# Performance work log

Hardware: AMD Instinct MI355X
Metric: run time of the kernel (lower is better)

The kernel has to match this reference:

```python
import jax, jax.numpy as jnp
import numpy as np

# MLA config (must match init_kwargs)
D_MODEL = 2048
NUM_HEADS = 16
HEAD_DIM = D_MODEL // NUM_HEADS          # 128
D_LATENT = 512
D_QK = D_LATENT // 2                      # 256
D_V = D_LATENT - D_QK                     # 256
ROPE_DIM = 64
QK_DEC = HEAD_DIM - ROPE_DIM              # 64
B, S = 2, 2048


def _glorot(key, shape):
    lim = np.sqrt(6.0 / (shape[0] + shape[1]))
    return jax.random.uniform(key, shape, jnp.float32, -lim, lim)


def setup_inputs() -> dict:
    key = jax.random.key(0)
    ks = jax.random.split(key, 8)
    return {
        "x": jax.random.normal(ks[0], (B, S, D_MODEL), jnp.float32),
        "W_comp": _glorot(ks[1], (D_MODEL, D_LATENT)),
        "W_q_dec": _glorot(ks[2], (D_QK, NUM_HEADS * QK_DEC)),
        "W_k_dec": _glorot(ks[3], (D_QK, NUM_HEADS * QK_DEC)),
        "W_v_dec": _glorot(ks[4], (D_V, NUM_HEADS * HEAD_DIM)),
        "W_rope_q": _glorot(ks[5], (D_MODEL, NUM_HEADS * ROPE_DIM)),
        "W_rope_k": _glorot(ks[6], (D_MODEL, NUM_HEADS * ROPE_DIM)),
        "W_out": _glorot(ks[7], (D_MODEL, D_MODEL)),
    }


def _apply_rope(t):
    # t: [B, S, H, ROPE_DIM]; rotate-half formulation with base 10000
    half = ROPE_DIM // 2
    inv_freq = 1.0 / (10000.0 ** (jnp.arange(0, ROPE_DIM, 2, dtype=jnp.float32) / ROPE_DIM))
    ang = jnp.arange(t.shape[1], dtype=jnp.float32)[:, None] * inv_freq[None, :]  # [S, half]
    cos = jnp.cos(ang)[None, :, None, :]
    sin = jnp.sin(ang)[None, :, None, :]
    t1, t2 = t[..., :half], t[..., half:]
    return jnp.concatenate([t1 * cos - t2 * sin, t1 * sin + t2 * cos], axis=-1)


def reference(x, W_comp, W_q_dec, W_k_dec, W_v_dec, W_rope_q, W_rope_k, W_out):
    # Compress to shared latent [B,S,d_latent]
    compressed = jnp.einsum("bsd,dl->bsl", x, W_comp)
    c_qk = compressed[:, :, :D_QK]
    c_v = compressed[:, :, D_QK:]

    # Decompress content parts and project RoPE parts from raw input
    q_no_rope = jnp.einsum("bsl,lh->bsh", c_qk, W_q_dec)   # [B,S,H*QK_DEC]
    k_no_rope = jnp.einsum("bsl,lh->bsh", c_qk, W_k_dec)
    v = jnp.einsum("bsl,lh->bsh", c_v, W_v_dec).reshape(B, S, NUM_HEADS, HEAD_DIM)
    q_rope = jnp.einsum("bsd,dh->bsh", x, W_rope_q)        # [B,S,H*ROPE_DIM]
    k_rope = jnp.einsum("bsd,dh->bsh", x, W_rope_k)

    # Faithful to source: concat along flat feature dim, then reshape to heads
    q = jnp.concatenate([q_no_rope, q_rope], axis=-1).reshape(B, S, NUM_HEADS, HEAD_DIM)
    k = jnp.concatenate([k_no_rope, k_rope], axis=-1).reshape(B, S, NUM_HEADS, HEAD_DIM)

    # Apply RoPE to last ROPE_DIM dims of each head
    q = jnp.concatenate([q[..., :QK_DEC], _apply_rope(q[..., QK_DEC:])], axis=-1)
    k = jnp.concatenate([k[..., :QK_DEC], _apply_rope(k[..., QK_DEC:])], axis=-1)

    scale = 1.0 / jnp.sqrt(jnp.float32(HEAD_DIM))
    scores = jnp.einsum("bqhd,bkhd->bhqk", q, k) * scale   # [B,H,S,S]
    attn = jax.nn.softmax(scores, axis=-1)
    ctx = jnp.einsum("bhqk,bkhd->bqhd", attn, v).reshape(B, S, D_MODEL)
    return jnp.einsum("bsd,de->bse", ctx, W_out)
```

## Files before the change

### kernel.cpp

```cpp
#include <hip/hip_runtime.h>
#include <stdint.h>

typedef __bf16 bf16x8 __attribute__((ext_vector_type(8)));
typedef __bf16 bf16x4 __attribute__((ext_vector_type(4)));
typedef float f32x4 __attribute__((ext_vector_type(4)));
typedef float f32x16 __attribute__((ext_vector_type(16)));

constexpr int NB   = 2;
constexpr int SEQ  = 2048;
constexpr int DM   = 2048;
constexpr int NH   = 16;
constexpr int HD   = 128;
constexpr int DL   = 512;
constexpr int ROWS = NB * SEQ;

__device__ __forceinline__ void gload16(const void* g, void* l) {
  __builtin_amdgcn_global_load_lds((const __attribute__((address_space(1))) uint32_t*)(const void*)g,
                                   (__attribute__((address_space(3))) uint32_t*)(void*)l, 16, 0, 0);
}

__device__ __forceinline__ uint32_t pk2(float lo, float hi) {
  union { __bf16 h[2]; uint32_t u; } x;
  x.h[0] = (__bf16)lo; x.h[1] = (__bf16)hi;
  return x.u;
}

__global__ __launch_bounds__(256) void cast_bf16(const float* __restrict__ in,
                                                 __bf16* __restrict__ out, int n4) {
  int i = blockIdx.x * blockDim.x + threadIdx.x;
  int stride = gridDim.x * blockDim.x;
  for (int k = i; k < n4; k += stride) {
    float4 v = ((const float4*)in)[k];
    union { __bf16 h[4]; uint2 u; } uo;
    uo.h[0] = (__bf16)v.x; uo.h[1] = (__bf16)v.y;
    uo.h[2] = (__bf16)v.z; uo.h[3] = (__bf16)v.w;
    ((uint2*)out)[k] = uo.u;
  }
}

__global__ __launch_bounds__(256) void transpose_cast(const float* __restrict__ in,
                                                      __bf16* __restrict__ out,
                                                      int R, int C) {
  __shared__ float t[32][33];
  int r0 = blockIdx.y * 32, c0 = blockIdx.x * 32;
  int tx = threadIdx.x, ty = threadIdx.y;
#pragma unroll
  for (int i = 0; i < 4; ++i)
    t[ty + 8*i][tx] = in[(size_t)(r0 + ty + 8*i) * C + c0 + tx];
  __syncthreads();
#pragma unroll
  for (int i = 0; i < 4; ++i)
    out[(size_t)(c0 + ty + 8*i) * R + r0 + tx] = (__bf16)t[tx][ty + 8*i];
}

__global__ __launch_bounds__(256) void transpose_v(const __bf16* __restrict__ v,
                                                   __bf16* __restrict__ vt) {
  __shared__ __bf16 t[32][33];
  int b = blockIdx.z >> 4, h = blockIdx.z & 15;
  int s0 = blockIdx.x * 32, d0 = blockIdx.y * 32;
  int tx = threadIdx.x, ty = threadIdx.y;
#pragma unroll
  for (int i = 0; i < 4; ++i)
    t[ty + 8*i][tx] = v[(size_t)(b*SEQ + s0 + ty + 8*i) * 2048 + h*128 + d0 + tx];
  __syncthreads();
#pragma unroll
  for (int i = 0; i < 4; ++i)
    vt[((size_t)(b*NH + h) * 128 + d0 + ty + 8*i) * 2048 + s0 + tx] = t[tx][ty + 8*i];
}

template <typename CT>
__global__ __launch_bounds__(256) void gemm_bt(const __bf16* __restrict__ A, int lda,
                                               const __bf16* __restrict__ Bt, int ldb,
                                               CT* __restrict__ C, int ldc, int K_) {
  __shared__ __align__(16) __bf16 As[128 * 32];
  __shared__ __align__(16) __bf16 Bs[128 * 32];
  const int m0 = blockIdx.y * 128, n0 = blockIdx.x * 128;
  const int t = threadIdx.x;
  const int wid = t >> 6, lane = t & 63;
  const int wr = (wid >> 1) * 64, wc = (wid & 1) * 64;
  const int lr = lane & 15, lg = lane >> 4;
  f32x4 acc[4][4] = {};
  for (int k0 = 0; k0 < K_; k0 += 32) {
    __syncthreads();
#pragma unroll
    for (int j = 0; j < 2; ++j) {
      int ob = j * 4096 + wid * 1024;
      int o  = ob + lane * 16;
      int row = o >> 6, colb = o & 63;
      gload16((const char*)A  + ((size_t)(m0 + row) * lda + k0) * 2 + colb, (char*)As + ob);
      gload16((const char*)Bt + ((size_t)(n0 + row) * ldb + k0) * 2 + colb, (char*)Bs + ob);
    }
    __syncthreads();
    bf16x8 af[4], bfr[4];
#pragma unroll
    for (int mi = 0; mi < 4; ++mi)
      af[mi] = *(const bf16x8*)(As + (wr + mi*16 + lr) * 32 + 8*lg);
#pragma unroll
    for (int ni = 0; ni < 4; ++ni)
      bfr[ni] = *(const bf16x8*)(Bs + (wc + ni*16 + lr) * 32 + 8*lg);
#pragma unroll
    for (int mi = 0; mi < 4; ++mi)
#pragma unroll
      for (int ni = 0; ni < 4; ++ni)
        acc[mi][ni] = __builtin_amdgcn_mfma_f32_16x16x32_bf16(af[mi], bfr[ni], acc[mi][ni], 0, 0, 0);
  }
#pragma unroll
  for (int mi = 0; mi < 4; ++mi)
#pragma unroll
    for (int ni = 0; ni < 4; ++ni) {
      int r = m0 + wr + mi*16 + lg*4;
      int c = n0 + wc + ni*16 + lr;
#pragma unroll
      for (int j = 0; j < 4; ++j)
        C[(size_t)(r + j) * ldc + c] = (CT)acc[mi][ni][j];
    }
}

__global__ __launch_bounds__(64) void rope_assemble(const __bf16* __restrict__ nr,
                                                    const __bf16* __restrict__ rp,
                                                    __bf16* __restrict__ full) {
  int idx = blockIdx.x;
  int h = idx & 15, bs = idx >> 4;
  int s = bs & (SEQ - 1);
  int j = threadIdx.x;
  const size_t ibase = (size_t)bs * 1024;
  const size_t obase = (size_t)bs * 2048 + h * 128;
  auto get = [&](int d) -> float {
    int flat = h * 128 + d;
    return (flat < 1024) ? (float)nr[ibase + flat] : (float)rp[ibase + flat - 1024];
  };
  full[obase + j] = (__bf16)get(j);
  if (j < 32) {
    float t1 = get(64 + j), t2 = get(96 + j);
    float inv = exp2f(-0.41524101186092029f * (float)j);
    float ang = (float)s * inv;
    float sn, cs;
    sincosf(ang, &sn, &cs);
    full[obase + 64 + j] = (__bf16)(t1 * cs - t2 * sn);
    full[obase + 96 + j] = (__bf16)(t1 * sn + t2 * cs);
  }
}

__global__ __launch_bounds__(256, 2) void attn_fwd(const __bf16* __restrict__ qf,
                                                   const __bf16* __restrict__ kf,
                                                   const __bf16* __restrict__ vt,
                                                   __bf16* __restrict__ ctx) {
  __shared__ __align__(16) char Ks[2][16384];
  __shared__ __align__(16) char Vs[2][16384];
  const int t = threadIdx.x;
  const int wid = t >> 6, lane = t & 63;
  const int lq = lane & 31, hi = lane >> 5;
  const int h = blockIdx.y, b = blockIdx.z;
  const int qrow = blockIdx.x * 128 + wid * 32 + lq;
  const char* kbh = (const char*)(kf + (size_t)b * SEQ * DM + h * HD);
  const char* vbh = (const char*)(vt + (size_t)(b * NH + h) * HD * SEQ);

  bf16x8 qfr[8];
  const __bf16* qrp = qf + (size_t)(b * SEQ + qrow) * DM + h * HD;
#pragma unroll
  for (int kk = 0; kk < 8; ++kk)
    qfr[kk] = *(const bf16x8*)(qrp + kk * 16 + 8 * hi);

  f32x16 accO[4] = {};
  float mrun = -1e30f, lsum = 0.f;
  const float scale = 0.088388347648318447f;

  auto stageK = [&](int buf, int kc) {
#pragma unroll
    for (int i = 0; i < 4; ++i) {
      int ob = wid * 4096 + i * 1024;
      int o  = ob + lane * 16;
      int key = o >> 8, sb = o & 255;
      int cb  = sb ^ ((key & 7) << 4);
      gload16(kbh + (size_t)(kc + key) * (DM * 2) + cb, Ks[buf] + ob);
    }
  };
  auto stageV = [&](int buf, int kc) {
#pragma unroll
    for (int i = 0; i < 4; ++i) {
      int ob = wid * 4096 + i * 1024;
      int o  = ob + lane * 16;
      int d = o >> 7, sb = o & 127;
      int cb = sb ^ ((d & 7) << 4);
      gload16(vbh + (size_t)d * (SEQ * 2) + (size_t)kc * 2 + cb, Vs[buf] + ob);
    }
  };

  stageK(0, 0); stageV(0, 0);
  __syncthreads();
  int cur = 0;
  for (int kc = 0; kc < SEQ; kc += 64) {
    if (kc + 64 < SEQ) { stageK(cur ^ 1, kc + 64); stageV(cur ^ 1, kc + 64); }

    f32x16 st[2] = {};
#pragma unroll
    for (int tt = 0; tt < 2; ++tt) {
      const int key = tt * 32 + lq;
      const char* kb = Ks[cur] + key * 256;
      const int swz = (key & 7) << 4;
#pragma unroll
      for (int kk = 0; kk < 8; ++kk) {
        bf16x8 kfr = *(const bf16x8*)(kb + ((32 * kk + 16 * hi) ^ swz));
        st[tt] = __builtin_amdgcn_mfma_f32_32x32x16_bf16(kfr, qfr[kk], st[tt], 0, 0, 0);
      }
    }

    float p[2][16];
    float cmax = -1e30f;
#pragma unroll
    for (int tt = 0; tt < 2; ++tt)
#pragma unroll
      for (int r = 0; r < 16; ++r) {
        float v = st[tt][r] * scale;
        p[tt][r] = v;
        cmax = fmaxf(cmax, v);
      }
    cmax = fmaxf(cmax, __shfl_xor(cmax, 32));
    float mnew = fmaxf(mrun, cmax);
    float corr = __expf(mrun - mnew);
    float psum = 0.f;
#pragma unroll
    for (int tt = 0; tt < 2; ++tt)
#pragma unroll
      for (int r = 0; r < 16; ++r) {
        p[tt][r] = __expf(p[tt][r] - mnew);
        psum += p[tt][r];
      }
    psum += __shfl_xor(psum, 32);
    lsum = lsum * corr + psum;
    mrun = mnew;
#pragma unroll
    for (int db = 0; db < 4; ++db) accO[db] *= corr;

    bf16x8 pfrag[4];
#pragma unroll
    for (int sl = 0; sl < 4; ++sl) {
      const int tt = sl >> 1, kk = sl & 1;
      uint32_t a0 = pk2(p[tt][8*kk + 0], p[tt][8*kk + 1]);
      uint32_t a1 = pk2(p[tt][8*kk + 2], p[tt][8*kk + 3]);
      uint32_t b0 = pk2(p[tt][8*kk + 4], p[tt][8*kk + 5]);
      uint32_t b1 = pk2(p[tt][8*kk + 6], p[tt][8*kk + 7]);
      uint32_t pa0 = (uint32_t)__shfl_xor((int)a0, 32);
      uint32_t pa1 = (uint32_t)__shfl_xor((int)a1, 32);
      uint32_t pb0 = (uint32_t)__shfl_xor((int)b0, 32);
      uint32_t pb1 = (uint32_t)__shfl_xor((int)b1, 32);
      union { uint32_t u[4]; bf16x8 v; } pu;
      pu.u[0] = hi ? pb0 : a0;
      pu.u[1] = hi ? pb1 : a1;
      pu.u[2] = hi ? b0 : pa0;
      pu.u[3] = hi ? b1 : pa1;
      pfrag[sl] = pu.v;
    }

#pragma unroll
    for (int db = 0; db < 4; ++db) {
      const int d = db * 32 + lq;
      const char* vb = Vs[cur] + d * 128;
      const int swz = (d & 7) << 4;
#pragma unroll
      for (int sl = 0; sl < 4; ++sl) {
        bf16x8 vfr = *(const bf16x8*)(vb + ((32 * sl + 16 * hi) ^ swz));
        accO[db] = __builtin_amdgcn_mfma_f32_32x32x16_bf16(vfr, pfrag[sl], accO[db], 0, 0, 0);
      }
    }
    __syncthreads();
    cur ^= 1;
  }

  float inv = 1.f / lsum;
  __bf16* op = ctx + (size_t)(b * SEQ + qrow) * DM + h * HD;
#pragma unroll
  for (int db = 0; db < 4; ++db)
#pragma unroll
    for (int a = 0; a < 4; ++a) {
      bf16x4 o4;
#pragma unroll
      for (int j = 0; j < 4; ++j) o4[j] = (__bf16)(accO[db][4*a + j] * inv);
      *(bf16x4*)(op + db*32 + 8*a + 4*hi) = o4;
    }
}

extern "C" void kernel_launch(void* const* d_in, const int* in_sizes, int n_in,
                              void* d_out, int out_size, void* d_ws, size_t ws_size,
                              hipStream_t stream) {
  const float* x   = (const float*)d_in[0];
  const float* Wc  = (const float*)d_in[1];
  const float* Wq  = (const float*)d_in[2];
  const float* Wk  = (const float*)d_in[3];
  const float* Wv  = (const float*)d_in[4];
  const float* Wrq = (const float*)d_in[5];
  const float* Wrk = (const float*)d_in[6];
  const float* Wo  = (const float*)d_in[7];
  float* out = (float*)d_out;

  char* ws = (char*)d_ws;
  size_t off = 0;
  auto take = [&](size_t bytes) { char* p = ws + off; off += bytes; return (__bf16*)p; };
  __bf16* xb    = take((size_t)ROWS * DM * 2);
  __bf16* comp  = take((size_t)ROWS * DL * 2);
  __bf16* qnr   = take((size_t)ROWS * 1024 * 2);
  __bf16* knr   = take((size_t)ROWS * 1024 * 2);
  __bf16* qr    = take((size_t)ROWS * 1024 * 2);
  __bf16* kr    = take((size_t)ROWS * 1024 * 2);
  __bf16* vb    = take((size_t)ROWS * 2048 * 2);
  __bf16* qfull = take((size_t)ROWS * 2048 * 2);
  __bf16* kfull = take((size_t)ROWS * 2048 * 2);
  __bf16* WcT   = take((size_t)512 * 2048 * 2);
  __bf16* WqT   = take((size_t)1024 * 256 * 2);
  __bf16* WkT   = take((size_t)1024 * 256 * 2);
  __bf16* WvT   = take((size_t)2048 * 256 * 2);
  __bf16* WrqT  = take((size_t)1024 * 2048 * 2);
  __bf16* WrkT  = take((size_t)1024 * 2048 * 2);
  __bf16* WoT   = take((size_t)2048 * 2048 * 2);
  __bf16* ctx = qnr;
  __bf16* vtr = qr;

  dim3 tb(32, 8);
  cast_bf16<<<4096, 256, 0, stream>>>(x, xb, ROWS * DM / 4);
  transpose_cast<<<dim3(512/32,  2048/32), tb, 0, stream>>>(Wc,  WcT,  2048, 512);
  transpose_cast<<<dim3(1024/32, 256/32),  tb, 0, stream>>>(Wq,  WqT,  256, 1024);
  transpose_cast<<<dim3(1024/32, 256/32),  tb, 0, stream>>>(Wk,  WkT,  256, 1024);
  transpose_cast<<<dim3(2048/32, 256/32),  tb, 0, stream>>>(Wv,  WvT,  256, 2048);
  transpose_cast<<<dim3(1024/32, 2048/32), tb, 0, stream>>>(Wrq, WrqT, 2048, 1024);
  transpose_cast<<<dim3(1024/32, 2048/32), tb, 0, stream>>>(Wrk, WrkT, 2048, 1024);
  transpose_cast<<<dim3(2048/32, 2048/32), tb, 0, stream>>>(Wo,  WoT,  2048, 2048);

  gemm_bt<__bf16><<<dim3(512/128, ROWS/128), 256, 0, stream>>>(xb, DM, WcT, DM, comp, DL, DM);
  gemm_bt<__bf16><<<dim3(1024/128, ROWS/128), 256, 0, stream>>>(xb, DM, WrqT, DM, qr, 1024, DM);
  gemm_bt<__bf16><<<dim3(1024/128, ROWS/128), 256, 0, stream>>>(xb, DM, WrkT, DM, kr, 1024, DM);
  gemm_bt<__bf16><<<dim3(1024/128, ROWS/128), 256, 0, stream>>>(comp, DL, WqT, 256, qnr, 1024, 256);
  gemm_bt<__bf16><<<dim3(1024/128, ROWS/128), 256, 0, stream>>>(comp, DL, WkT, 256, knr, 1024, 256);
  gemm_bt<__bf16><<<dim3(2048/128, ROWS/128), 256, 0, stream>>>(comp + 256, DL, WvT, 256, vb, 2048, 256);

  rope_assemble<<<ROWS * NH, 64, 0, stream>>>(qnr, qr, qfull);
  rope_assemble<<<ROWS * NH, 64, 0, stream>>>(knr, kr, kfull);
  transpose_v<<<dim3(SEQ/32, 128/32, NB*NH), tb, 0, stream>>>(vb, vtr);

  attn_fwd<<<dim3(SEQ/128, NH, NB), 256, 0, stream>>>(qfull, kfull, vtr, ctx);

  gemm_bt<float><<<dim3(2048/128, ROWS/128), 256, 0, stream>>>(ctx, DM, WoT, DM, out, 2048, DM);
}
```

Before: 500.2 us.

## Merge Q/K projection GEMMs, swizzle GEMM tiles, vectorize RoPE, lazy softmax rescale

Doubles the GEMM K-step to 64 and adds an XOR swizzle on the LDS tiles to reduce bank conflicts and per-step barrier overhead. The paired q/k projection GEMMs are merged into single wider launches by relying on the adjacent workspace layout of the weight and output buffers. RoPE assembly now handles a whole row per block with vectorized 8-wide loads, shares sin/cos through LDS, and folds the softmax scale into Q. The attention kernel only rescales its accumulators when the running max grows by more than a threshold, and raises wave priority around the MFMA sections. Merging depends on implicit buffer contiguity, and the lazy rescale lets exponent values grow up to e^8 before rescaling.

Result: faster. 403.6 us (-19.3%).

```diff
diff --git a/kernel.cpp b/kernel.cpp
--- a/kernel.cpp
+++ b/kernel.cpp
@@ -72,37 +72,45 @@
 __global__ __launch_bounds__(256) void gemm_bt(const __bf16* __restrict__ A, int lda,
                                                const __bf16* __restrict__ Bt, int ldb,
                                                CT* __restrict__ C, int ldc, int K_) {
-  __shared__ __align__(16) __bf16 As[128 * 32];
-  __shared__ __align__(16) __bf16 Bs[128 * 32];
+  __shared__ __align__(16) char As[16384];
+  __shared__ __align__(16) char Bs[16384];
   const int m0 = blockIdx.y * 128, n0 = blockIdx.x * 128;
   const int t = threadIdx.x;
   const int wid = t >> 6, lane = t & 63;
   const int wr = (wid >> 1) * 64, wc = (wid & 1) * 64;
   const int lr = lane & 15, lg = lane >> 4;
   f32x4 acc[4][4] = {};
-  for (int k0 = 0; k0 < K_; k0 += 32) {
+  for (int k0 = 0; k0 < K_; k0 += 64) {
     __syncthreads();
 #pragma unroll
-    for (int j = 0; j < 2; ++j) {
-      int ob = j * 4096 + wid * 1024;
-      int o  = ob + lane * 16;
-      int row = o >> 6, colb = o & 63;
-      gload16((const char*)A  + ((size_t)(m0 + row) * lda + k0) * 2 + colb, (char*)As + ob);
-      gload16((const char*)Bt + ((size_t)(n0 + row) * ldb + k0) * 2 + colb, (char*)Bs + ob);
+    for (int i = 0; i < 4; ++i) {
+      int obi = wid * 4096 + i * 1024;
+      int o   = obi + lane * 16;
+      int row = o >> 7, sb = o & 127;
+      int cb  = sb ^ ((row & 7) << 4);
+      gload16((const char*)A  + ((size_t)(m0 + row) * lda + k0) * 2 + cb, As + obi);
+      gload16((const char*)Bt + ((size_t)(n0 + row) * ldb + k0) * 2 + cb, Bs + obi);
     }
     __syncthreads();
-    bf16x8 af[4], bfr[4];
-#pragma unroll
-    for (int mi = 0; mi < 4; ++mi)
-      af[mi] = *(const bf16x8*)(As + (wr + mi*16 + lr) * 32 + 8*lg);
-#pragma unroll
-    for (int ni = 0; ni < 4; ++ni)
-      bfr[ni] = *(const bf16x8*)(Bs + (wc + ni*16 + lr) * 32 + 8*lg);
-#pragma unroll
-    for (int mi = 0; mi < 4; ++mi)
-#pragma unroll
-      for (int ni = 0; ni < 4; ++ni)
-        acc[mi][ni] = __builtin_amdgcn_mfma_f32_16x16x32_bf16(af[mi], bfr[ni], acc[mi][ni], 0, 0, 0);
+#pragma unroll
+    for (int kk = 0; kk < 2; ++kk) {
+      bf16x8 af[4], bfr[4];
+#pragma unroll
+      for (int mi = 0; mi < 4; ++mi) {
+        int row = wr + mi*16 + lr;
+        af[mi] = *(const bf16x8*)(As + row * 128 + ((kk*64 + 16*lg) ^ ((row & 7) << 4)));
+      }
+#pragma unroll
+      for (int ni = 0; ni < 4; ++ni) {
+        int row = wc + ni*16 + lr;
+        bfr[ni] = *(const bf16x8*)(Bs + row * 128 + ((kk*64 + 16*lg) ^ ((row & 7) << 4)));
+      }
+#pragma unroll
+      for (int mi = 0; mi < 4; ++mi)
+#pragma unroll
+        for (int ni = 0; ni < 4; ++ni)
+          acc[mi][ni] = __builtin_amdgcn_mfma_f32_16x16x32_bf16(af[mi], bfr[ni], acc[mi][ni], 0, 0, 0);
+    }
   }
 #pragma unroll
   for (int mi = 0; mi < 4; ++mi)
@@ -116,29 +124,47 @@
     }
 }
 
-__global__ __launch_bounds__(64) void rope_assemble(const __bf16* __restrict__ nr,
-                                                    const __bf16* __restrict__ rp,
-                                                    __bf16* __restrict__ full) {
-  int idx = blockIdx.x;
-  int h = idx & 15, bs = idx >> 4;
-  int s = bs & (SEQ - 1);
-  int j = threadIdx.x;
-  const size_t ibase = (size_t)bs * 1024;
-  const size_t obase = (size_t)bs * 2048 + h * 128;
-  auto get = [&](int d) -> float {
-    int flat = h * 128 + d;
-    return (flat < 1024) ? (float)nr[ibase + flat] : (float)rp[ibase + flat - 1024];
-  };
-  full[obase + j] = (__bf16)get(j);
-  if (j < 32) {
-    float t1 = get(64 + j), t2 = get(96 + j);
-    float inv = exp2f(-0.41524101186092029f * (float)j);
+__global__ __launch_bounds__(256) void rope_assemble(const __bf16* __restrict__ nr,
+                                                     const __bf16* __restrict__ rp,
+                                                     int ld, __bf16* __restrict__ full,
+                                                     float SC) {
+  __shared__ float cs[32], sn[32];
+  const int bs = blockIdx.x;
+  const int s = bs & (SEQ - 1);
+  const int t = threadIdx.x;
+  if (t < 32) {
+    float inv = exp2f(-0.41524101186092029f * (float)t);
     float ang = (float)s * inv;
-    float sn, cs;
-    sincosf(ang, &sn, &cs);
-    full[obase + 64 + j] = (__bf16)(t1 * cs - t2 * sn);
-    full[obase + 96 + j] = (__bf16)(t1 * sn + t2 * cs);
-  }
+    sincosf(ang, &sn[t], &cs[t]);
+  }
+  __syncthreads();
+  const __bf16* nrow = nr + (size_t)bs * ld;
+  const __bf16* rrow = rp + (size_t)bs * ld;
+  __bf16* orow = full + (size_t)bs * 2048;
+  const int c0 = t * 8;
+  const __bf16* src = (c0 < 1024) ? (nrow + c0) : (rrow + (c0 - 1024));
+  const int dh = c0 & 127;
+  bf16x8 v = *(const bf16x8*)src;
+  bf16x8 o;
+  if (dh < 64) {
+#pragma unroll
+    for (int i = 0; i < 8; ++i) o[i] = (__bf16)((float)v[i] * SC);
+  } else if (dh < 96) {
+    bf16x8 v2 = *(const bf16x8*)(src + 32);
+#pragma unroll
+    for (int i = 0; i < 8; ++i) {
+      int j = dh - 64 + i;
+      o[i] = (__bf16)(((float)v[i] * cs[j] - (float)v2[i] * sn[j]) * SC);
+    }
+  } else {
+    bf16x8 v1 = *(const bf16x8*)(src - 32);
+#pragma unroll
+    for (int i = 0; i < 8; ++i) {
+      int j = dh - 96 + i;
+      o[i] = (__bf16)(((float)v1[i] * sn[j] + (float)v[i] * cs[j]) * SC);
+    }
+  }
+  *(bf16x8*)(orow + c0) = o;
 }
 
 __global__ __launch_bounds__(256, 2) void attn_fwd(const __bf16* __restrict__ qf,
@@ -163,7 +189,6 @@
 
   f32x16 accO[4] = {};
   float mrun = -1e30f, lsum = 0.f;
-  const float scale = 0.088388347648318447f;
 
   auto stageK = [&](int buf, int kc) {
 #pragma unroll
@@ -193,6 +218,7 @@
     if (kc + 64 < SEQ) { stageK(cur ^ 1, kc + 64); stageV(cur ^ 1, kc + 64); }
 
     f32x16 st[2] = {};
+    __builtin_amdgcn_s_setprio(1);
 #pragma unroll
     for (int tt = 0; tt < 2; ++tt) {
       const int key = tt * 32 + lq;
@@ -204,6 +230,7 @@
         st[tt] = __builtin_amdgcn_mfma_f32_32x32x16_bf16(kfr, qfr[kk], st[tt], 0, 0, 0);
       }
     }
+    __builtin_amdgcn_s_setprio(0);
 
     float p[2][16];
     float cmax = -1e30f;
@@ -211,26 +238,28 @@
     for (int tt = 0; tt < 2; ++tt)
 #pragma unroll
       for (int r = 0; r < 16; ++r) {
-        float v = st[tt][r] * scale;
-        p[tt][r] = v;
-        cmax = fmaxf(cmax, v);
+        p[tt][r] = st[tt][r];
+        cmax = fmaxf(cmax, st[tt][r]);
       }
     cmax = fmaxf(cmax, __shfl_xor(cmax, 32));
-    float mnew = fmaxf(mrun, cmax);
-    float corr = __expf(mrun - mnew);
+    if (!__all(cmax - mrun <= 8.f)) {
+      float mnew = fmaxf(mrun, cmax);
+      float corr = __expf(mrun - mnew);
+      lsum *= corr;
+#pragma unroll
+      for (int db = 0; db < 4; ++db) accO[db] *= corr;
+      mrun = mnew;
+    }
     float psum = 0.f;
 #pragma unroll
     for (int tt = 0; tt < 2; ++tt)
 #pragma unroll
       for (int r = 0; r < 16; ++r) {
-        p[tt][r] = __expf(p[tt][r] - mnew);
+        p[tt][r] = __expf(p[tt][r] - mrun);
         psum += p[tt][r];
       }
     psum += __shfl_xor(psum, 32);
-    lsum = lsum * corr + psum;
-    mrun = mnew;
-#pragma unroll
-    for (int db = 0; db < 4; ++db) accO[db] *= corr;
+    lsum += psum;
 
     bf16x8 pfrag[4];
 #pragma unroll
@@ -252,6 +281,7 @@
       pfrag[sl] = pu.v;
     }
 
+    __builtin_amdgcn_s_setprio(1);
 #pragma unroll
     for (int db = 0; db < 4; ++db) {
       const int d = db * 32 + lq;
@@ -263,6 +293,7 @@
         accO[db] = __builtin_amdgcn_mfma_f32_32x32x16_bf16(vfr, pfrag[sl], accO[db], 0, 0, 0);
       }
     }
+    __builtin_amdgcn_s_setprio(0);
     __syncthreads();
     cur ^= 1;
   }
@@ -312,8 +343,11 @@
   __bf16* WrqT  = take((size_t)1024 * 2048 * 2);
   __bf16* WrkT  = take((size_t)1024 * 2048 * 2);
   __bf16* WoT   = take((size_t)2048 * 2048 * 2);
+  (void)knr; (void)kr; (void)WkT; (void)WrkT;
   __bf16* ctx = qnr;
   __bf16* vtr = qr;
+
+  const float scale = 0.088388347648318447f;
 
   dim3 tb(32, 8);
   cast_bf16<<<4096, 256, 0, stream>>>(x, xb, ROWS * DM / 4);
@@ -326,14 +360,12 @@
   transpose_cast<<<dim3(2048/32, 2048/32), tb, 0, stream>>>(Wo,  WoT,  2048, 2048);
 
   gemm_bt<__bf16><<<dim3(512/128, ROWS/128), 256, 0, stream>>>(xb, DM, WcT, DM, comp, DL, DM);
-  gemm_bt<__bf16><<<dim3(1024/128, ROWS/128), 256, 0, stream>>>(xb, DM, WrqT, DM, qr, 1024, DM);
-  gemm_bt<__bf16><<<dim3(1024/128, ROWS/128), 256, 0, stream>>>(xb, DM, WrkT, DM, kr, 1024, DM);
-  gemm_bt<__bf16><<<dim3(1024/128, ROWS/128), 256, 0, stream>>>(comp, DL, WqT, 256, qnr, 1024, 256);
-  gemm_bt<__bf16><<<dim3(1024/128, ROWS/128), 256, 0, stream>>>(comp, DL, WkT, 256, knr, 1024, 256);
+  gemm_bt<__bf16><<<dim3(2048/128, ROWS/128), 256, 0, stream>>>(xb, DM, WrqT, DM, qr, 2048, DM);
+  gemm_bt<__bf16><<<dim3(2048/128, ROWS/128), 256, 0, stream>>>(comp, DL, WqT, 256, qnr, 2048, 256);
   gemm_bt<__bf16><<<dim3(2048/128, ROWS/128), 256, 0, stream>>>(comp + 256, DL, WvT, 256, vb, 2048, 256);
 
-  rope_assemble<<<ROWS * NH, 64, 0, stream>>>(qnr, qr, qfull);
-  rope_assemble<<<ROWS * NH, 64, 0, stream>>>(knr, kr, kfull);
+  rope_assemble<<<ROWS, 256, 0, stream>>>(qnr,        qr,        2048, qfull, scale);
+  rope_assemble<<<ROWS, 256, 0, stream>>>(qnr + 1024, qr + 1024, 2048, kfull, 1.0f);
   transpose_v<<<dim3(SEQ/32, 128/32, NB*NH), tb, 0, stream>>>(vb, vtr);
 
   attn_fwd<<<dim3(SEQ/128, NH, NB), 256, 0, stream>>>(qfull, kfull, vtr, ctx);
```
